# Performance work log

Hardware: AMD Instinct MI355X
Metric: run time of the kernel (lower is better)

## Reference

```python
import jax, jax.numpy as jnp
import numpy as np

# Large finite negative used for masking inside the softmax chain. exp(NEG - m)
# underflows to exactly 0.0 in fp32, so valid positions match the torch -inf
# masking bit-for-bit; masked output positions are set to -inf at the end.
NEG = jnp.float32(-1e30)

B, L, F = 8192, 128, 64


def setup_inputs() -> dict:
    key = jax.random.key(0)
    k1, k2, k3 = jax.random.split(key, 3)
    return {
        "choice_set_features": jax.random.normal(k1, (B, L, F), dtype=jnp.float32),
        "choice_set_lengths": jax.random.randint(k2, (B,), 1, L + 1),  # in [1, L]
        "thetas": jax.random.uniform(k3, (F, F), dtype=jnp.float32),   # torch.rand init
        "mixture_weights": jnp.ones((F,), dtype=jnp.float32),
    }


def reference(choice_set_features, choice_set_lengths, thetas, mixture_weights):
    b, l, f = choice_set_features.shape
    # utilities[b,l,g] = x[b,l,:] @ thetas[g,:]   (x @ thetas.T)
    util = jnp.einsum('blf,gf->blg', choice_set_features, thetas)
    pad = jnp.arange(l)[None, :] >= choice_set_lengths[:, None]  # [B, L] True = padded
    util = jnp.where(pad[..., None], NEG, util)
    # log_softmax over the choice-set dimension (dim 1), per mixture component
    log_probs = jax.nn.log_softmax(util, axis=1)
    # mixture over components (dim 2) with log-softmaxed mixture weights
    out = jax.nn.logsumexp(log_probs + jax.nn.log_softmax(mixture_weights), axis=2)
    # padded slots are exactly -inf in the torch reference
    return jnp.where(pad, -jnp.inf, out)
```

## Files before the change

kernel.cpp:

```cpp
#include <hip/hip_runtime.h>
#include <math.h>

#define NEGV  (-1e30f)
#define LOG2E 1.44269504088896340736f
#define LN2   0.69314718055994530942f

typedef __attribute__((ext_vector_type(8))) _Float16 half8;
typedef __attribute__((ext_vector_type(2))) __fp16   fp16x2;
typedef __attribute__((ext_vector_type(4))) float f32x4;

__device__ __forceinline__ float exp2_fast(float a) { return __builtin_amdgcn_exp2f(a); }
__device__ __forceinline__ float log2_fast(float a) { return __builtin_amdgcn_logf(a); }

__device__ __forceinline__ half8 cvt8(float4 a, float4 b) {
    union { half8 v; fp16x2 p[4]; } u;
    u.p[0] = __builtin_amdgcn_cvt_pkrtz(a.x, a.y);
    u.p[1] = __builtin_amdgcn_cvt_pkrtz(a.z, a.w);
    u.p[2] = __builtin_amdgcn_cvt_pkrtz(b.x, b.y);
    u.p[3] = __builtin_amdgcn_cvt_pkrtz(b.z, b.w);
    return u.v;
}

#define WS_FLOATS_NEEDED (64 + 8 * 64 * 4)

__global__ void prep_kernel(const float* __restrict__ theta,
                            const float* __restrict__ mw,
                            float* __restrict__ ws)
{
    const int lane = threadIdx.x;
    const int c15  = lane & 15;
    const int q    = lane >> 4;

    const float v = mw[lane];
    float m = v;
#pragma unroll
    for (int s = 32; s >= 1; s >>= 1) m = fmaxf(m, __shfl_xor(m, s, 64));
    float e = __expf(v - m);
#pragma unroll
    for (int s = 32; s >= 1; s >>= 1) e += __shfl_xor(e, s, 64);
    const float logZ = m + __logf(e);
    ws[lane] = (v - logZ) * LOG2E;

#pragma unroll
    for (int w = 0; w < 4; ++w) {
        const float* tr = theta + (size_t)((w << 4) + c15) * 64 + (q << 3);
#pragma unroll
        for (int kt = 0; kt < 2; ++kt) {
            float4 a = *(const float4*)(tr + kt * 32);
            float4 c = *(const float4*)(tr + kt * 32 + 4);
            a.x *= LOG2E; a.y *= LOG2E; a.z *= LOG2E; a.w *= LOG2E;
            c.x *= LOG2E; c.y *= LOG2E; c.z *= LOG2E; c.w *= LOG2E;
            const half8 h = cvt8(a, c);
            const int s = (w << 1) + kt;
            *(half8*)&ws[64 + ((size_t)(s * 64 + lane)) * 4] = h;
        }
    }
}

template<bool USE_WS>
__global__ __launch_bounds__(256, 6) void mixed_logit_kernel(
    const float* __restrict__ x,
    const int*   __restrict__ lens,
    const float* __restrict__ theta,
    const float* __restrict__ mw,
    const float* __restrict__ ws,
    float* __restrict__ out)
{
    __shared__ __align__(16) unsigned char xbuf[128 * 144];
    __shared__ float red_s[4][128];

    const int tid  = threadIdx.x;
    const int lane = tid & 63;
    const int w    = tid >> 6;
    const int c15  = lane & 15;
    const int q    = lane >> 4;
    const int b    = blockIdx.x;
    const int len  = lens[b];

    half8 th[2];
    float wg[4];
    if constexpr (USE_WS) {
#pragma unroll
        for (int kt = 0; kt < 2; ++kt)
            th[kt] = *(const half8*)&ws[64 + ((size_t)((((w << 1) + kt) * 64) + lane)) * 4];
        const float4 wv = *(const float4*)&ws[(w << 4) + (q << 2)];
        wg[0] = wv.x; wg[1] = wv.y; wg[2] = wv.z; wg[3] = wv.w;
    } else {
        const float* tr = theta + (size_t)((w << 4) + c15) * 64 + (q << 3);
#pragma unroll
        for (int kt = 0; kt < 2; ++kt) {
            float4 a = *(const float4*)(tr + kt * 32);
            float4 c = *(const float4*)(tr + kt * 32 + 4);
            a.x *= LOG2E; a.y *= LOG2E; a.z *= LOG2E; a.w *= LOG2E;
            c.x *= LOG2E; c.y *= LOG2E; c.z *= LOG2E; c.w *= LOG2E;
            th[kt] = cvt8(a, c);
        }
        const float mwl = mw[lane];
        float mmax = mwl;
#pragma unroll
        for (int s = 32; s >= 1; s >>= 1) mmax = fmaxf(mmax, __shfl_xor(mmax, s, 64));
        float me = __expf(mwl - mmax);
#pragma unroll
        for (int s = 32; s >= 1; s >>= 1) me += __shfl_xor(me, s, 64);
        const float logZ = mmax + __logf(me);
#pragma unroll
        for (int i = 0; i < 4; ++i)
            wg[i] = (mw[(w << 4) + (q << 2) + i] - logZ) * LOG2E;
    }

    {
        const float4* xp = (const float4*)(x + (size_t)b * 8192);
        float4 ra[8];
#pragma unroll
        for (int i = 0; i < 4; ++i) {
            const int j2 = (i << 8) + tid;
            ra[2 * i]     = xp[j2 * 2];
            ra[2 * i + 1] = xp[j2 * 2 + 1];
        }
#pragma unroll
        for (int i = 0; i < 4; ++i) {
            const int j2 = (i << 8) + tid;
            const half8 h = cvt8(ra[2 * i], ra[2 * i + 1]);
            *(half8*)(xbuf + (j2 >> 3) * 144 + (j2 & 7) * 16) = h;
        }
    }
    __syncthreads();

    f32x4 acc[8];
#pragma unroll
    for (int nt = 0; nt < 8; ++nt) acc[nt] = (f32x4){0.f, 0.f, 0.f, 0.f};

#pragma unroll
    for (int nt = 0; nt < 8; ++nt) {
        const unsigned char* rb = xbuf + ((nt << 4) + c15) * 144 + (q << 4);
        const half8 x0 = *(const half8*)(rb);
        const half8 x1 = *(const half8*)(rb + 64);
        acc[nt] = __builtin_amdgcn_mfma_f32_16x16x32_f16(th[0], x0, acc[nt], 0, 0, 0);
        acc[nt] = __builtin_amdgcn_mfma_f32_16x16x32_f16(th[1], x1, acc[nt], 0, 0, 0);
    }

#pragma unroll
    for (int nt = 0; nt < 8; ++nt) {
        const bool v = ((nt << 4) + c15) < len;
#pragma unroll
        for (int i = 0; i < 4; ++i) acc[nt][i] = v ? acc[nt][i] : NEGV;
    }

    float c4[4];
#pragma unroll
    for (int i = 0; i < 4; ++i) {
        float e = 0.f;
#pragma unroll
        for (int nt = 0; nt < 8; ++nt) e += exp2_fast(acc[nt][i]);
#pragma unroll
        for (int s = 1; s < 16; s <<= 1) e += __shfl_xor(e, s, 64);
        c4[i] = wg[i] - log2_fast(e);
    }

#pragma unroll
    for (int nt = 0; nt < 8; ++nt) {
        float s2 = exp2_fast(acc[nt][0] + c4[0]) + exp2_fast(acc[nt][1] + c4[1])
                 + exp2_fast(acc[nt][2] + c4[2]) + exp2_fast(acc[nt][3] + c4[3]);
        s2 += __shfl_xor(s2, 16, 64);
        s2 += __shfl_xor(s2, 32, 64);
        if ((nt >> 1) == q) {
            red_s[w][(nt << 4) + c15] = s2;
        }
    }
    __syncthreads();

    if (tid < 128) {
        const int l = tid;
        const float S = red_s[0][l] + red_s[1][l] + red_s[2][l] + red_s[3][l];
        const float o = LN2 * log2_fast(S);
        out[(size_t)b * 128 + l] = (l < len) ? o : NEGV;
    }
}

extern "C" void kernel_launch(void* const* d_in, const int* in_sizes, int n_in,
                              void* d_out, int out_size, void* d_ws, size_t ws_size,
                              hipStream_t stream) {
    const float* x     = (const float*)d_in[0];
    const int*   lens  = (const int*)d_in[1];
    const float* theta = (const float*)d_in[2];
    const float* mw    = (const float*)d_in[3];
    float* out = (float*)d_out;
    const int B = in_sizes[1];

    if (ws_size >= (size_t)WS_FLOATS_NEEDED * sizeof(float)) {
        float* ws = (float*)d_ws;
        prep_kernel<<<1, 64, 0, stream>>>(theta, mw, ws);
        mixed_logit_kernel<true><<<B, 256, 0, stream>>>(x, lens, theta, mw, ws, out);
    } else {
        mixed_logit_kernel<false><<<B, 256, 0, stream>>>(x, lens, theta, mw, nullptr, out);
    }
}
```

Before: 49.54 us.

## Split choice-set rows across waves and load x directly into MFMA registers

Each wave now owns 32 rows of the choice set and computes all 64 mixture components for them, instead of one 16-component slice over all 128 rows. Each wave loads its x rows straight from global memory into fp16 MFMA operands, so the LDS staging copy of x goes away. The cross-row softmax denominators are built through a partial-sum exchange in LDS, and the final mixture reduction stays inside the wave. The cost is more theta registers per thread (4x2 half8) and a lower occupancy hint in launch_bounds, from 6 down to 4.

```diff
diff --git a/kernel.cpp b/kernel.cpp
--- a/kernel.cpp
+++ b/kernel.cpp
@@ -42,8 +42,8 @@
     ws[lane] = (v - logZ) * LOG2E;
 
 #pragma unroll
-    for (int w = 0; w < 4; ++w) {
-        const float* tr = theta + (size_t)((w << 4) + c15) * 64 + (q << 3);
+    for (int gt = 0; gt < 4; ++gt) {
+        const float* tr = theta + (size_t)((gt << 4) + c15) * 64 + (q << 3);
 #pragma unroll
         for (int kt = 0; kt < 2; ++kt) {
             float4 a = *(const float4*)(tr + kt * 32);
@@ -51,14 +51,14 @@
             a.x *= LOG2E; a.y *= LOG2E; a.z *= LOG2E; a.w *= LOG2E;
             c.x *= LOG2E; c.y *= LOG2E; c.z *= LOG2E; c.w *= LOG2E;
             const half8 h = cvt8(a, c);
-            const int s = (w << 1) + kt;
+            const int s = (gt << 1) + kt;
             *(half8*)&ws[64 + ((size_t)(s * 64 + lane)) * 4] = h;
         }
     }
 }
 
 template<bool USE_WS>
-__global__ __launch_bounds__(256, 6) void mixed_logit_kernel(
+__global__ __launch_bounds__(256, 4) void mixed_logit_kernel(
     const float* __restrict__ x,
     const int*   __restrict__ lens,
     const float* __restrict__ theta,
@@ -66,8 +66,8 @@
     const float* __restrict__ ws,
     float* __restrict__ out)
 {
-    __shared__ __align__(16) unsigned char xbuf[128 * 144];
-    __shared__ float red_s[4][128];
+    __shared__ __align__(16) unsigned char lds_p[64 * 272];
+    __shared__ __align__(16) float lds_c[64];
 
     const int tid  = threadIdx.x;
     const int lane = tid & 63;
@@ -77,23 +77,26 @@
     const int b    = blockIdx.x;
     const int len  = lens[b];
 
-    half8 th[2];
-    float wg[4];
+    half8 th[4][2];
+    float logZ_fb = 0.f;
     if constexpr (USE_WS) {
 #pragma unroll
-        for (int kt = 0; kt < 2; ++kt)
-            th[kt] = *(const half8*)&ws[64 + ((size_t)((((w << 1) + kt) * 64) + lane)) * 4];
-        const float4 wv = *(const float4*)&ws[(w << 4) + (q << 2)];
-        wg[0] = wv.x; wg[1] = wv.y; wg[2] = wv.z; wg[3] = wv.w;
+        for (int gt = 0; gt < 4; ++gt)
+#pragma unroll
+            for (int kt = 0; kt < 2; ++kt)
+                th[gt][kt] = *(const half8*)&ws[64 + ((size_t)((((gt << 1) + kt) * 64) + lane)) * 4];
     } else {
-        const float* tr = theta + (size_t)((w << 4) + c15) * 64 + (q << 3);
-#pragma unroll
-        for (int kt = 0; kt < 2; ++kt) {
-            float4 a = *(const float4*)(tr + kt * 32);
-            float4 c = *(const float4*)(tr + kt * 32 + 4);
-            a.x *= LOG2E; a.y *= LOG2E; a.z *= LOG2E; a.w *= LOG2E;
-            c.x *= LOG2E; c.y *= LOG2E; c.z *= LOG2E; c.w *= LOG2E;
-            th[kt] = cvt8(a, c);
+#pragma unroll
+        for (int gt = 0; gt < 4; ++gt) {
+            const float* tr = theta + (size_t)((gt << 4) + c15) * 64 + (q << 3);
+#pragma unroll
+            for (int kt = 0; kt < 2; ++kt) {
+                float4 a = *(const float4*)(tr + kt * 32);
+                float4 c = *(const float4*)(tr + kt * 32 + 4);
+                a.x *= LOG2E; a.y *= LOG2E; a.z *= LOG2E; a.w *= LOG2E;
+                c.x *= LOG2E; c.y *= LOG2E; c.z *= LOG2E; c.w *= LOG2E;
+                th[gt][kt] = cvt8(a, c);
+            }
         }
         const float mwl = mw[lane];
         float mmax = mwl;
@@ -102,78 +105,104 @@
         float me = __expf(mwl - mmax);
 #pragma unroll
         for (int s = 32; s >= 1; s >>= 1) me += __shfl_xor(me, s, 64);
-        const float logZ = mmax + __logf(me);
-#pragma unroll
-        for (int i = 0; i < 4; ++i)
-            wg[i] = (mw[(w << 4) + (q << 2) + i] - logZ) * LOG2E;
-    }
-
-    {
-        const float4* xp = (const float4*)(x + (size_t)b * 8192);
-        float4 ra[8];
-#pragma unroll
-        for (int i = 0; i < 4; ++i) {
-            const int j2 = (i << 8) + tid;
-            ra[2 * i]     = xp[j2 * 2];
-            ra[2 * i + 1] = xp[j2 * 2 + 1];
-        }
-#pragma unroll
-        for (int i = 0; i < 4; ++i) {
-            const int j2 = (i << 8) + tid;
-            const half8 h = cvt8(ra[2 * i], ra[2 * i + 1]);
-            *(half8*)(xbuf + (j2 >> 3) * 144 + (j2 & 7) * 16) = h;
+        logZ_fb = mmax + __logf(me);
+    }
+
+    half8 xf[2][2];
+    {
+        const float* xb = x + (size_t)b * 8192;
+#pragma unroll
+        for (int lt_loc = 0; lt_loc < 2; ++lt_loc) {
+            const int row = (w << 5) + (lt_loc << 4) + c15;
+#pragma unroll
+            for (int kt = 0; kt < 2; ++kt) {
+                const float* p = xb + (size_t)row * 64 + kt * 32 + (q << 3);
+                xf[lt_loc][kt] = cvt8(*(const float4*)p, *(const float4*)(p + 4));
+            }
+        }
+    }
+
+    f32x4 acc[4][2];
+#pragma unroll
+    for (int gt = 0; gt < 4; ++gt)
+#pragma unroll
+        for (int lt = 0; lt < 2; ++lt) acc[gt][lt] = (f32x4){0.f, 0.f, 0.f, 0.f};
+
+#pragma unroll
+    for (int gt = 0; gt < 4; ++gt)
+#pragma unroll
+        for (int lt = 0; lt < 2; ++lt)
+#pragma unroll
+            for (int kt = 0; kt < 2; ++kt)
+                acc[gt][lt] = __builtin_amdgcn_mfma_f32_16x16x32_f16(th[gt][kt], xf[lt][kt], acc[gt][lt], 0, 0, 0);
+
+    {
+        const int l0 = (w << 5) + c15;
+        const bool v0 = l0 < len;
+        const bool v1 = (l0 + 16) < len;
+#pragma unroll
+        for (int gt = 0; gt < 4; ++gt)
+#pragma unroll
+            for (int i = 0; i < 4; ++i) {
+                acc[gt][0][i] = v0 ? acc[gt][0][i] : NEGV;
+                acc[gt][1][i] = v1 ? acc[gt][1][i] : NEGV;
+            }
+    }
+
+    {
+        unsigned char* base = lds_p + ((w << 4) + c15) * 272 + (q << 4);
+#pragma unroll
+        for (int gt = 0; gt < 4; ++gt) {
+            f32x4 p1;
+#pragma unroll
+            for (int i = 0; i < 4; ++i)
+                p1[i] = exp2_fast(acc[gt][0][i]) + exp2_fast(acc[gt][1][i]);
+            *(f32x4*)(base + (gt << 6)) = p1;
         }
     }
     __syncthreads();
 
-    f32x4 acc[8];
-#pragma unroll
-    for (int nt = 0; nt < 8; ++nt) acc[nt] = (f32x4){0.f, 0.f, 0.f, 0.f};
-
-#pragma unroll
-    for (int nt = 0; nt < 8; ++nt) {
-        const unsigned char* rb = xbuf + ((nt << 4) + c15) * 144 + (q << 4);
-        const half8 x0 = *(const half8*)(rb);
-        const half8 x1 = *(const half8*)(rb + 64);
-        acc[nt] = __builtin_amdgcn_mfma_f32_16x16x32_f16(th[0], x0, acc[nt], 0, 0, 0);
-        acc[nt] = __builtin_amdgcn_mfma_f32_16x16x32_f16(th[1], x1, acc[nt], 0, 0, 0);
-    }
-
-#pragma unroll
-    for (int nt = 0; nt < 8; ++nt) {
-        const bool v = ((nt << 4) + c15) < len;
-#pragma unroll
-        for (int i = 0; i < 4; ++i) acc[nt][i] = v ? acc[nt][i] : NEGV;
-    }
-
-    float c4[4];
-#pragma unroll
-    for (int i = 0; i < 4; ++i) {
-        float e = 0.f;
-#pragma unroll
-        for (int nt = 0; nt < 8; ++nt) e += exp2_fast(acc[nt][i]);
-#pragma unroll
-        for (int s = 1; s < 16; s <<= 1) e += __shfl_xor(e, s, 64);
-        c4[i] = wg[i] - log2_fast(e);
-    }
-
-#pragma unroll
-    for (int nt = 0; nt < 8; ++nt) {
-        float s2 = exp2_fast(acc[nt][0] + c4[0]) + exp2_fast(acc[nt][1] + c4[1])
-                 + exp2_fast(acc[nt][2] + c4[2]) + exp2_fast(acc[nt][3] + c4[3]);
-        s2 += __shfl_xor(s2, 16, 64);
-        s2 += __shfl_xor(s2, 32, 64);
-        if ((nt >> 1) == q) {
-            red_s[w][(nt << 4) + c15] = s2;
+    {
+        const int gg = (w << 4) + (lane >> 2);
+        const int r4 = lane & 3;
+        float s = 0.f;
+#pragma unroll
+        for (int k = 0; k < 16; ++k) {
+            const int rr = (r4 << 4) + ((k + (r4 << 2)) & 15);
+            s += *(const float*)(lds_p + rr * 272 + (gg << 2));
+        }
+        s += __shfl_xor(s, 1, 64);
+        s += __shfl_xor(s, 2, 64);
+        if (r4 == 0) {
+            float wgv;
+            if constexpr (USE_WS) wgv = ws[gg];
+            else                  wgv = (mw[gg] - logZ_fb) * LOG2E;
+            lds_c[gg] = wgv - log2_fast(s);
         }
     }
     __syncthreads();
 
-    if (tid < 128) {
-        const int l = tid;
-        const float S = red_s[0][l] + red_s[1][l] + red_s[2][l] + red_s[3][l];
-        const float o = LN2 * log2_fast(S);
-        out[(size_t)b * 128 + l] = (l < len) ? o : NEGV;
+    {
+        f32x4 c4[4];
+#pragma unroll
+        for (int gt = 0; gt < 4; ++gt)
+            c4[gt] = *(const f32x4*)((const unsigned char*)lds_c + (gt << 6) + (q << 4));
+
+#pragma unroll
+        for (int lt = 0; lt < 2; ++lt) {
+            float s2 = 0.f;
+#pragma unroll
+            for (int gt = 0; gt < 4; ++gt)
+#pragma unroll
+                for (int i = 0; i < 4; ++i)
+                    s2 += exp2_fast(acc[gt][lt][i] + c4[gt][i]);
+            s2 += __shfl_xor(s2, 16, 64);
+            s2 += __shfl_xor(s2, 32, 64);
+            if (q == 0) {
+                const int l = (w << 5) + (lt << 4) + c15;
+                out[(size_t)b * 128 + l] = (l < len) ? LN2 * log2_fast(s2) : NEGV;
+            }
+        }
     }
 }
 
```

Result: slower. 53.13 us (+7.3%).
